# Optimization experiments

Measured on AMD Instinct MI355X. Metric: run time of the kernel, lower is better.

Reference implementation:

```python
import jax, jax.numpy as jnp
import numpy as np

B, L, E, D, T, NS, NSYM = 1024, 80, 256, 256, 20, 4, 100


def setup_inputs() -> dict:
    key = jax.random.key(0)
    ks = jax.random.split(key, 20)
    s = 0.05  # weight scale
    inp = {
        "encoder_outputs": jax.random.normal(ks[0], (B, L, E), jnp.float32),
        "symbols_encodings": jax.random.normal(ks[1], (B, NSYM, D), jnp.float32),
        "target_symbols_idxs": jax.random.randint(ks[2], (B, T), 0, NS + NSYM),
        "common_emb": jax.random.normal(ks[3], (NS, D), jnp.float32) * s,
        "W_attn": jax.random.normal(ks[4], (L, 2 * D), jnp.float32) * s,
        "b_attn": jnp.zeros((L,), jnp.float32),
        "W_comb": jax.random.normal(ks[5], (D, D + E), jnp.float32) * s,
        "b_comb": jnp.zeros((D,), jnp.float32),
        "Wih0": jax.random.normal(ks[6], (4 * D, D), jnp.float32) * s,
        "Whh0": jax.random.normal(ks[7], (4 * D, D), jnp.float32) * s,
        "bih0": jnp.zeros((4 * D,), jnp.float32),
        "bhh0": jnp.zeros((4 * D,), jnp.float32),
        "Wih1": jax.random.normal(ks[8], (4 * D, D), jnp.float32) * s,
        "Whh1": jax.random.normal(ks[9], (4 * D, D), jnp.float32) * s,
        "bih1": jnp.zeros((4 * D,), jnp.float32),
        "bhh1": jnp.zeros((4 * D,), jnp.float32),
        "W_out": jax.random.normal(ks[10], (D, E), jnp.float32) * s,
        "b_out": jnp.zeros((D,), jnp.float32),
    }
    return inp


def _lstm_cell(x, h, c, Wih, Whh, bih, bhh):
    # PyTorch gate order: i, f, g, o
    g = x @ Wih.T + h @ Whh.T + bih + bhh
    i, f, gg, o = jnp.split(g, 4, axis=-1)
    c = jax.nn.sigmoid(f) * c + jax.nn.sigmoid(i) * jnp.tanh(gg)
    h = jax.nn.sigmoid(o) * jnp.tanh(c)
    return h, c


def reference(encoder_outputs, symbols_encodings, target_symbols_idxs,
              common_emb, W_attn, b_attn, W_comb, b_comb,
              Wih0, Whh0, bih0, bhh0, Wih1, Whh1, bih1, bhh1,
              W_out, b_out):
    b, t = target_symbols_idxs.shape
    ns = common_emb.shape[0]
    nsym = symbols_encodings.shape[1]
    dt = encoder_outputs.dtype
    d = symbols_encodings.shape[-1]

    # apply_batched_embeddings: idx < ns -> common table, else per-example table
    idx = target_symbols_idxs
    special = common_emb[jnp.clip(idx, 0, ns - 1)]                      # [B,T,D]
    batched = jnp.take_along_axis(
        symbols_encodings, jnp.clip(idx - ns, 0, nsym - 1)[..., None], axis=1)  # [B,T,D]
    emb = jnp.where((idx < ns)[..., None], special, batched)            # [B,T,D]
    emb_t = jnp.swapaxes(emb, 0, 1)                                     # [T,B,D]

    def step(carry, e):
        h0, c0, h1, c1 = carry
        # Bahdanau-style attention over encoder positions
        aw = jnp.concatenate([e, h1], axis=1) @ W_attn.T + b_attn       # [B,L]
        ap = jax.nn.softmax(aw, axis=1)
        applied = jnp.einsum('bl,ble->be', ap, encoder_outputs)         # [B,E]
        comb = jax.nn.relu(jnp.concatenate([e, applied], axis=1) @ W_comb.T + b_comb)
        h0, c0 = _lstm_cell(comb, h0, c0, Wih0, Whh0, bih0, bhh0)
        h1, c1 = _lstm_cell(h0, h1, c1, Wih1, Whh1, bih1, bhh1)
        out = jax.nn.log_softmax(h1 @ W_out.T + b_out, axis=1)          # [B,D]
        return (h0, c0, h1, c1), out

    init = tuple(jnp.zeros((b, d), dt) for _ in range(4))
    _, outs = jax.lax.scan(step, init, emb_t)
    return outs  # [T,B,D] stacked per-timestep log-probs
```

## Files before the change

kernel.cpp:

```cpp
#include <hip/hip_runtime.h>

#define B_ 1024
#define L_ 80
#define E_ 256
#define D_ 256
#define T_ 20
#define NS_ 4
#define NSYM_ 100

typedef __attribute__((ext_vector_type(8))) short short8;
typedef __attribute__((ext_vector_type(4))) float f32x4;

__device__ inline short f2b(float f) {
    unsigned u = __float_as_uint(f);
    unsigned r = (u + 0x7fffu + ((u >> 16) & 1u)) >> 16;
    return (short)r;
}
__device__ inline float b2f(short s) {
    return __uint_as_float(((unsigned)(unsigned short)s) << 16);
}


__global__ void zero_k(unsigned* __restrict__ p, size_t n) {
    size_t i = (size_t)blockIdx.x * blockDim.x + threadIdx.x;
    size_t stride = (size_t)gridDim.x * blockDim.x;
    for (; i < n; i += stride) p[i] = 0u;
}

__global__ void f2b4_k(const float* __restrict__ src, short* __restrict__ dst, size_t n4) {
    size_t i = (size_t)blockIdx.x * blockDim.x + threadIdx.x;
    size_t stride = (size_t)gridDim.x * blockDim.x;
    for (; i < n4; i += stride) {
        float4 v = ((const float4*)src)[i];
        short4 o;
        o.x = f2b(v.x); o.y = f2b(v.y); o.z = f2b(v.z); o.w = f2b(v.w);
        ((short4*)dst)[i] = o;
    }
}

__global__ void split_k(const float* __restrict__ Wsrc, short* __restrict__ dstE,
                        short* __restrict__ dstH, int rows) {
    int id = blockIdx.x * 256 + threadIdx.x;
    if (id >= rows * 512) return;
    int rr = id >> 9, cc = id & 511;
    short v = f2b(Wsrc[id]);
    if (cc < 256) dstE[rr * 256 + cc] = v;
    else          dstH[rr * 256 + (cc - 256)] = v;
}

__global__ void gatesW_k(const float* __restrict__ Wih, const float* __restrict__ Whh,
                         const float* __restrict__ bih, const float* __restrict__ bhh,
                         short* __restrict__ WgB, float* __restrict__ bg) {
    int id = blockIdx.x * 256 + threadIdx.x;
    int np = id >> 9, cc = id & 511;
    int u = np >> 2, g = np & 3;
    int srow = g * 256 + u;
    float v = (cc < 256) ? Wih[srow * 256 + cc] : Whh[srow * 256 + (cc - 256)];
    WgB[id] = f2b(v);
    if (id < 1024) {
        int u2 = id >> 2, g2 = id & 3;
        bg[id] = bih[g2 * 256 + u2] + bhh[g2 * 256 + u2];
    }
}

__global__ void embed_k(const int* __restrict__ tsi, const float* __restrict__ common,
                        const float* __restrict__ syms, short* __restrict__ embB) {
    size_t id = (size_t)blockIdx.x * 256 + threadIdx.x;
    int d = (int)(id & 255);
    size_t r = id >> 8;
    int tt = (int)(r >> 10);
    int b  = (int)(r & 1023);
    int idx = tsi[b * T_ + tt];
    float v;
    if (idx < NS_) {
        int i2 = idx < 0 ? 0 : idx;
        v = common[i2 * D_ + d];
    } else {
        int i2 = idx - NS_;
        if (i2 > NSYM_ - 1) i2 = NSYM_ - 1;
        v = syms[((size_t)b * NSYM_ + i2) * D_ + d];
    }
    embB[id] = f2b(v);
}


__global__ __launch_bounds__(256) void gemm_k(
    const short* __restrict__ A, int lda,
    const short* __restrict__ W,
    const float* __restrict__ addend, int ldAdd,
    const float* __restrict__ bias,
    int act,
    float* __restrict__ outF, int ldoF,
    short* __restrict__ outB, int ldoB,
    int M, int N, int K)
{
    __shared__ alignas(16) short As[64][40];
    __shared__ alignas(16) short Ws[64][40];
    int m0 = blockIdx.x * 64, n0 = blockIdx.y * 64;
    int t = threadIdx.x;
    int w = t >> 6, l = t & 63, quad = l >> 4, lm = l & 15;
    int wm = (w >> 1) * 32, wn = (w & 1) * 32;
    f32x4 acc[2][2] = {};
    int rowL = t >> 2, c8 = (t & 3) * 8;
    for (int k0 = 0; k0 < K; k0 += 32) {
        uint4 av = *(const uint4*)(A + (size_t)(m0 + rowL) * lda + k0 + c8);
        uint4 wv = {0u, 0u, 0u, 0u};
        int wr = n0 + rowL;
        if (wr < N) wv = *(const uint4*)(W + (size_t)wr * K + k0 + c8);
        *(uint4*)&As[rowL][c8] = av;
        *(uint4*)&Ws[rowL][c8] = wv;
        __syncthreads();
        short8 af[2], wf[2];
        af[0] = *(const short8*)&As[wm + lm][quad * 8];
        af[1] = *(const short8*)&As[wm + 16 + lm][quad * 8];
        wf[0] = *(const short8*)&Ws[wn + lm][quad * 8];
        wf[1] = *(const short8*)&Ws[wn + 16 + lm][quad * 8];
        #pragma unroll
        for (int i = 0; i < 2; i++)
            #pragma unroll
            for (int j = 0; j < 2; j++)
                acc[i][j] = __builtin_amdgcn_mfma_f32_16x16x32_bf16(af[i], wf[j], acc[i][j], 0, 0, 0);
        __syncthreads();
    }
    #pragma unroll
    for (int i = 0; i < 2; i++)
        #pragma unroll
        for (int j = 0; j < 2; j++) {
            int col = n0 + wn + j * 16 + lm;
            if (col >= N) continue;
            float bval = bias ? bias[col] : 0.f;
            #pragma unroll
            for (int r = 0; r < 4; r++) {
                int row = m0 + wm + i * 16 + quad * 4 + r;
                float v = acc[i][j][r] + bval;
                if (addend) v += addend[(size_t)row * ldAdd + col];
                if (act == 1) v = fmaxf(v, 0.f);
                if (outF) outF[(size_t)row * ldoF + col] = v;
                if (outB) outB[(size_t)row * ldoB + col] = f2b(v);
            }
        }
}


__global__ __launch_bounds__(256) void fused_attn_comb_k(
    const short* __restrict__ h1B,
    const short* __restrict__ WaH,
    const float* __restrict__ awEt,
    const short* __restrict__ encW,
    const float* __restrict__ combEt,
    const float* __restrict__ b_comb,
    short* __restrict__ X0p)
{
    __shared__ float h1S[256];
    __shared__ float awS[80];
    __shared__ float apS[80];
    int b = blockIdx.x, t = threadIdx.x;
    h1S[t] = b2f(h1B[(size_t)b * 256 + t]);
    __syncthreads();
    float aw = 0.f;
    if (t < 80) {
        const short8* wp = (const short8*)(WaH + (size_t)t * 256);
        float acc = 0.f;
        #pragma unroll 4
        for (int k = 0; k < 32; k++) {
            short8 wv = wp[k];
            const float* hp = &h1S[k * 8];
            acc += hp[0] * b2f(wv[0]) + hp[1] * b2f(wv[1])
                 + hp[2] * b2f(wv[2]) + hp[3] * b2f(wv[3])
                 + hp[4] * b2f(wv[4]) + hp[5] * b2f(wv[5])
                 + hp[6] * b2f(wv[6]) + hp[7] * b2f(wv[7]);
        }
        aw = acc + awEt[(size_t)b * 80 + t];
        awS[t] = aw;
    }
    __syncthreads();
    float mx = -1e30f;
    #pragma unroll 8
    for (int i = 0; i < 80; i++) mx = fmaxf(mx, awS[i]);
    if (t < 80) apS[t] = __expf(aw - mx);
    __syncthreads();
    float s = 0.f;
    #pragma unroll 8
    for (int i = 0; i < 80; i++) s += apS[i];
    float inv = 1.f / s;
    const short* p = encW + (size_t)b * 80 * 256 + t;
    float acc = 0.f;
    #pragma unroll 8
    for (int l = 0; l < 80; l++) acc += apS[l] * b2f(p[(size_t)l * 256]);
    float v = acc * inv + combEt[(size_t)b * 256 + t] + b_comb[t];
    v = fmaxf(v, 0.f);
    X0p[(size_t)b * 512 + t] = f2b(v);
}


__global__ __launch_bounds__(256) void gates_lstm_k(
    const short* __restrict__ X,
    const short* __restrict__ Wg,
    const float* __restrict__ bg,
    float* __restrict__ c,
    short* __restrict__ hA, int ldA, int offA,
    short* __restrict__ hB2, int ldB2, int offB2)
{
    __shared__ alignas(16) short As[64][40];
    __shared__ alignas(16) short Ws[64][40];
    __shared__ float gS[64][68];
    int m0 = blockIdx.x * 64, n0 = blockIdx.y * 64;
    int t = threadIdx.x, w = t >> 6, l = t & 63, quad = l >> 4, lm = l & 15;
    int wm = (w >> 1) * 32, wn = (w & 1) * 32;
    f32x4 acc[2][2] = {};
    int rowL = t >> 2, c8 = (t & 3) * 8;
    for (int k0 = 0; k0 < 512; k0 += 32) {
        *(uint4*)&As[rowL][c8] = *(const uint4*)(X + (size_t)(m0 + rowL) * 512 + k0 + c8);
        *(uint4*)&Ws[rowL][c8] = *(const uint4*)(Wg + (size_t)(n0 + rowL) * 512 + k0 + c8);
        __syncthreads();
        short8 af[2], wf[2];
        af[0] = *(const short8*)&As[wm + lm][quad * 8];
        af[1] = *(const short8*)&As[wm + 16 + lm][quad * 8];
        wf[0] = *(const short8*)&Ws[wn + lm][quad * 8];
        wf[1] = *(const short8*)&Ws[wn + 16 + lm][quad * 8];
        #pragma unroll
        for (int i = 0; i < 2; i++)
            #pragma unroll
            for (int j = 0; j < 2; j++)
                acc[i][j] = __builtin_amdgcn_mfma_f32_16x16x32_bf16(af[i], wf[j], acc[i][j], 0, 0, 0);
        __syncthreads();
    }
    #pragma unroll
    for (int i = 0; i < 2; i++)
        #pragma unroll
        for (int j = 0; j < 2; j++) {
            int col = wn + j * 16 + lm;
            float bval = bg[n0 + col];
            #pragma unroll
            for (int r = 0; r < 4; r++)
                gS[wm + i * 16 + quad * 4 + r][col] = acc[i][j][r] + bval;
        }
    __syncthreads();
    int U0 = n0 >> 2;
    for (int item = t; item < 1024; item += 256) {
        int ml = item >> 4, ul = item & 15;
        float iv = gS[ml][ul * 4 + 0];
        float fv = gS[ml][ul * 4 + 1];
        float gv = gS[ml][ul * 4 + 2];
        float ov = gS[ml][ul * 4 + 3];
        float si = 1.f / (1.f + __expf(-iv));
        float sf = 1.f / (1.f + __expf(-fv));
        float so = 1.f / (1.f + __expf(-ov));
        float tg = tanhf(gv);
        int m = m0 + ml, u = U0 + ul;
        size_t ci = (size_t)m * 256 + u;
        float cn = sf * c[ci] + si * tg;
        float hn = so * tanhf(cn);
        c[ci] = cn;
        short hb = f2b(hn);
        hA[(size_t)m * ldA + offA + u] = hb;
        hB2[(size_t)m * ldB2 + offB2 + u] = hb;
    }
}


__global__ __launch_bounds__(256) void out_k(
    const short* __restrict__ h1B,
    const short* __restrict__ WoB,
    const float* __restrict__ b_out,
    float* __restrict__ outT)
{
    __shared__ alignas(16) short As[32][40];
    __shared__ alignas(16) short Ws[256][40];
    __shared__ float oS[32][260];
    int m0 = blockIdx.x * 32;
    int t = threadIdx.x, w = t >> 6, l = t & 63, quad = l >> 4, lm = l & 15;
    int wm = (w >> 1) * 16, wn = (w & 1) * 128;
    f32x4 acc[8] = {};
    for (int k0 = 0; k0 < 256; k0 += 32) {
        if (t < 128) {
            int rr = t >> 2, cc = (t & 3) * 8;
            *(uint4*)&As[rr][cc] = *(const uint4*)(h1B + (size_t)(m0 + rr) * 256 + k0 + cc);
        }
        for (int cch = t; cch < 1024; cch += 256) {
            int rr = cch >> 2, cc = (cch & 3) * 8;
            *(uint4*)&Ws[rr][cc] = *(const uint4*)(WoB + (size_t)rr * 256 + k0 + cc);
        }
        __syncthreads();
        short8 af = *(const short8*)&As[wm + lm][quad * 8];
        #pragma unroll
        for (int j = 0; j < 8; j++) {
            short8 wf = *(const short8*)&Ws[wn + j * 16 + lm][quad * 8];
            acc[j] = __builtin_amdgcn_mfma_f32_16x16x32_bf16(af, wf, acc[j], 0, 0, 0);
        }
        __syncthreads();
    }
    #pragma unroll
    for (int j = 0; j < 8; j++)
        #pragma unroll
        for (int r = 0; r < 4; r++)
            oS[wm + quad * 4 + r][wn + j * 16 + lm] = acc[j][r] + b_out[wn + j * 16 + lm];
    __syncthreads();
    int row = t >> 3, q = t & 7;
    float mx = -1e30f;
    for (int i = q * 32; i < q * 32 + 32; i++) mx = fmaxf(mx, oS[row][i]);
    mx = fmaxf(mx, __shfl_xor(mx, 1));
    mx = fmaxf(mx, __shfl_xor(mx, 2));
    mx = fmaxf(mx, __shfl_xor(mx, 4));
    float s = 0.f;
    for (int i = q * 32; i < q * 32 + 32; i++) s += __expf(oS[row][i] - mx);
    s += __shfl_xor(s, 1); s += __shfl_xor(s, 2); s += __shfl_xor(s, 4);
    float lg = mx + logf(s);
    float* orow = outT + (size_t)(m0 + row) * 256;
    for (int i = q * 32; i < q * 32 + 32; i++) orow[i] = oS[row][i] - lg;
}


extern "C" void kernel_launch(void* const* d_in, const int* in_sizes, int n_in,
                              void* d_out, int out_size, void* d_ws, size_t ws_size,
                              hipStream_t stream) {
    const float* encF    = (const float*)d_in[0];
    const float* syms    = (const float*)d_in[1];
    const int*   tsi     = (const int*)d_in[2];
    const float* commonE = (const float*)d_in[3];
    const float* W_attn  = (const float*)d_in[4];
    const float* b_attn  = (const float*)d_in[5];
    const float* W_comb  = (const float*)d_in[6];
    const float* b_comb  = (const float*)d_in[7];
    const float* Wih0    = (const float*)d_in[8];
    const float* Whh0    = (const float*)d_in[9];
    const float* bih0    = (const float*)d_in[10];
    const float* bhh0    = (const float*)d_in[11];
    const float* Wih1    = (const float*)d_in[12];
    const float* Whh1    = (const float*)d_in[13];
    const float* bih1    = (const float*)d_in[14];
    const float* bhh1    = (const float*)d_in[15];
    const float* W_out   = (const float*)d_in[16];
    const float* b_out   = (const float*)d_in[17];
    float* out = (float*)d_out;

    char* base = (char*)d_ws;
    size_t off = 0;
    auto alloc = [&](size_t bytes) -> char* {
        char* p = base + off;
        off += (bytes + 255) & ~(size_t)255;
        return p;
    };
    float* c0    = (float*)alloc((size_t)B_ * D_ * 4);
    float* c1    = (float*)alloc((size_t)B_ * D_ * 4);
    short* X0a   = (short*)alloc((size_t)B_ * 512 * 2);
    short* X1a   = (short*)alloc((size_t)B_ * 512 * 2);
    short* H1all = (short*)alloc((size_t)(T_ + 1) * B_ * D_ * 2);
    size_t zeroBytes = (size_t)((char*)H1all - base) + (size_t)B_ * D_ * 2;
    short* X0b   = (short*)alloc((size_t)B_ * 512 * 2);
    short* X1b   = (short*)alloc((size_t)B_ * 512 * 2);
    float* awE   = (float*)alloc((size_t)T_ * B_ * L_ * 4);
    float* combE = (float*)alloc((size_t)T_ * B_ * D_ * 4);
    short* embB  = (short*)alloc((size_t)T_ * B_ * D_ * 2);
    short* WaEB  = (short*)alloc((size_t)L_ * D_ * 2);
    short* WaHB  = (short*)alloc((size_t)L_ * D_ * 2);
    short* WcEB  = (short*)alloc((size_t)D_ * D_ * 2);
    short* WcAB  = (short*)alloc((size_t)D_ * E_ * 2);
    short* Wg0B  = (short*)alloc((size_t)1024 * 512 * 2);
    short* Wg1B  = (short*)alloc((size_t)1024 * 512 * 2);
    short* WoutB = (short*)alloc((size_t)D_ * E_ * 2);
    float* bg0   = (float*)alloc(1024 * 4);
    float* bg1   = (float*)alloc(1024 * 4);
    short* encB  = (short*)alloc((size_t)B_ * L_ * E_ * 2);
    short* encW  = (short*)alloc((size_t)B_ * L_ * D_ * 2);
    (void)encF; (void)ws_size; (void)in_sizes; (void)n_in; (void)out_size;

    zero_k<<<2048, 256, 0, stream>>>((unsigned*)base, zeroBytes / 4);
    f2b4_k<<<4096, 256, 0, stream>>>(encF, encB, (size_t)B_ * L_ * E_ / 4);
    f2b4_k<<<64, 256, 0, stream>>>(W_out, WoutB, (size_t)D_ * E_ / 4);
    split_k<<<(80 * 512) / 256, 256, 0, stream>>>(W_attn, WaEB, WaHB, 80);
    split_k<<<(256 * 512) / 256, 256, 0, stream>>>(W_comb, WcEB, WcAB, 256);
    gatesW_k<<<2048, 256, 0, stream>>>(Wih0, Whh0, bih0, bhh0, Wg0B, bg0);
    gatesW_k<<<2048, 256, 0, stream>>>(Wih1, Whh1, bih1, bhh1, Wg1B, bg1);
    embed_k<<<(T_ * B_ * D_) / 256, 256, 0, stream>>>(tsi, commonE, syms, embB);
    gemm_k<<<dim3(320, 2), 256, 0, stream>>>(embB, 256, WaEB, nullptr, 0, b_attn, 0,
                                             awE, 80, nullptr, 0, 20480, 80, 256);
    gemm_k<<<dim3(320, 4), 256, 0, stream>>>(embB, 256, WcEB, nullptr, 0, nullptr, 0,
                                             combE, 256, nullptr, 0, 20480, 256, 256);
    gemm_k<<<dim3(1280, 4), 256, 0, stream>>>(encB, 256, WcAB, nullptr, 0, nullptr, 0,
                                              nullptr, 0, encW, 256, 81920, 256, 256);

    for (int tt = 0; tt < T_; tt++) {
        int p = tt & 1;
        short* X0p = p ? X0b : X0a;
        short* X0q = p ? X0a : X0b;
        short* X1p = p ? X1b : X1a;
        short* X1q = p ? X1a : X1b;

        fused_attn_comb_k<<<1024, 256, 0, stream>>>(
            H1all + (size_t)tt * B_ * D_, WaHB, awE + (size_t)tt * B_ * L_,
            encW, combE + (size_t)tt * B_ * D_, b_comb, X0p);
        gates_lstm_k<<<dim3(16, 16), 256, 0, stream>>>(X0p, Wg0B, bg0, c0,
                                                       X0q, 512, 256, X1p, 512, 0);
        gates_lstm_k<<<dim3(16, 16), 256, 0, stream>>>(X1p, Wg1B, bg1, c1,
                                                       X1q, 512, 256,
                                                       H1all + (size_t)(tt + 1) * B_ * D_, 256, 0);
    }
    out_k<<<640, 256, 0, stream>>>(H1all + (size_t)B_ * D_, WoutB, b_out, out);
}
```

Before: 1.082 ms.

## Fuse decoder time loop into one persistent kernel with on-chip LSTM state

Replaces the per-timestep launches (attention/combine plus two LSTM gate kernels, 60 launches) with one persistent kernel. Each of 64 blocks owns 16 batch rows for all 20 steps. The LSTM cell states stay in registers and the hidden and input vectors stay in LDS, so the global zeroing kernel and the intermediate round-trips through memory go away. The attention score projection now uses MFMA, and the comb bias is folded into the precomputed GEMM. The cost is that only 64 workgroups run, far fewer than the CUs available, and every block streams the full gate weight matrices from L2 at every step, so the kernel may become limited by per-CU bandwidth.

```diff
diff --git a/kernel.cpp b/kernel.cpp
--- a/kernel.cpp
+++ b/kernel.cpp
@@ -8,6 +8,11 @@
 #define NS_ 4
 #define NSYM_ 100
 
+#define ROWS 16
+#define NBLK 64
+#define XP 520
+#define GP 260
+
 typedef __attribute__((ext_vector_type(8))) short short8;
 typedef __attribute__((ext_vector_type(4))) float f32x4;
 
@@ -20,12 +25,6 @@
     return __uint_as_float(((unsigned)(unsigned short)s) << 16);
 }
 
-
-__global__ void zero_k(unsigned* __restrict__ p, size_t n) {
-    size_t i = (size_t)blockIdx.x * blockDim.x + threadIdx.x;
-    size_t stride = (size_t)gridDim.x * blockDim.x;
-    for (; i < n; i += stride) p[i] = 0u;
-}
 
 __global__ void f2b4_k(const float* __restrict__ src, short* __restrict__ dst, size_t n4) {
     size_t i = (size_t)blockIdx.x * blockDim.x + threadIdx.x;
@@ -142,119 +141,152 @@
 }
 
 
-__global__ __launch_bounds__(256) void fused_attn_comb_k(
-    const short* __restrict__ h1B,
-    const short* __restrict__ WaH,
-    const float* __restrict__ awEt,
-    const short* __restrict__ encW,
-    const float* __restrict__ combEt,
-    const float* __restrict__ b_comb,
-    short* __restrict__ X0p)
-{
-    __shared__ float h1S[256];
-    __shared__ float awS[80];
-    __shared__ float apS[80];
-    int b = blockIdx.x, t = threadIdx.x;
-    h1S[t] = b2f(h1B[(size_t)b * 256 + t]);
-    __syncthreads();
-    float aw = 0.f;
-    if (t < 80) {
-        const short8* wp = (const short8*)(WaH + (size_t)t * 256);
-        float acc = 0.f;
-        #pragma unroll 4
-        for (int k = 0; k < 32; k++) {
-            short8 wv = wp[k];
-            const float* hp = &h1S[k * 8];
-            acc += hp[0] * b2f(wv[0]) + hp[1] * b2f(wv[1])
-                 + hp[2] * b2f(wv[2]) + hp[3] * b2f(wv[3])
-                 + hp[4] * b2f(wv[4]) + hp[5] * b2f(wv[5])
-                 + hp[6] * b2f(wv[6]) + hp[7] * b2f(wv[7]);
-        }
-        aw = acc + awEt[(size_t)b * 80 + t];
-        awS[t] = aw;
-    }
-    __syncthreads();
-    float mx = -1e30f;
-    #pragma unroll 8
-    for (int i = 0; i < 80; i++) mx = fmaxf(mx, awS[i]);
-    if (t < 80) apS[t] = __expf(aw - mx);
-    __syncthreads();
-    float s = 0.f;
-    #pragma unroll 8
-    for (int i = 0; i < 80; i++) s += apS[i];
-    float inv = 1.f / s;
-    const short* p = encW + (size_t)b * 80 * 256 + t;
-    float acc = 0.f;
-    #pragma unroll 8
-    for (int l = 0; l < 80; l++) acc += apS[l] * b2f(p[(size_t)l * 256]);
-    float v = acc * inv + combEt[(size_t)b * 256 + t] + b_comb[t];
-    v = fmaxf(v, 0.f);
-    X0p[(size_t)b * 512 + t] = f2b(v);
-}
-
-
-__global__ __launch_bounds__(256) void gates_lstm_k(
-    const short* __restrict__ X,
+struct DecArgs {
+    short* H1all;
+    const short* WaHB;
+    const float* awE;
+    const short* encW;
+    const float* combE;
+    const short* Wg0; const float* bg0;
+    const short* Wg1; const float* bg1;
+};
+
+__device__ inline void layer_lstm(
+    const short (*X)[XP],
     const short* __restrict__ Wg,
     const float* __restrict__ bg,
-    float* __restrict__ c,
-    short* __restrict__ hA, int ldA, int offA,
-    short* __restrict__ hB2, int ldB2, int offB2)
+    float* creg,
+    float (*gSv)[GP],
+    short (*Hd1)[XP], int off1,
+    short (*Hd2)[XP], int off2,
+    short* __restrict__ gdst,
+    int w, int l, int quad, int lm)
 {
-    __shared__ alignas(16) short As[64][40];
-    __shared__ alignas(16) short Ws[64][40];
-    __shared__ float gS[64][68];
-    int m0 = blockIdx.x * 64, n0 = blockIdx.y * 64;
+    f32x4 acc[16] = {};
+    #pragma unroll 4
+    for (int k0s = 0; k0s < 16; k0s++) {
+        int k0 = k0s * 32;
+        short8 af = *(const short8*)&X[lm][k0 + quad * 8];
+        #pragma unroll
+        for (int j = 0; j < 16; j++) {
+            short8 wf = *(const short8*)(Wg + (size_t)(w * 256 + j * 16 + lm) * 512 + k0 + quad * 8);
+            acc[j] = __builtin_amdgcn_mfma_f32_16x16x32_bf16(af, wf, acc[j], 0, 0, 0);
+        }
+    }
+    __syncthreads();
+    #pragma unroll
+    for (int j = 0; j < 16; j++) {
+        float bv = bg[w * 256 + j * 16 + lm];
+        #pragma unroll
+        for (int r = 0; r < 4; r++)
+            gSv[quad * 4 + r][j * 16 + lm] = acc[j][r] + bv;
+    }
+    int u = w * 64 + l;
+    #pragma unroll
+    for (int row = 0; row < ROWS; row++) {
+        float4 g4 = *(const float4*)&gSv[row][l * 4];
+        float si = 1.f / (1.f + __expf(-g4.x));
+        float sf = 1.f / (1.f + __expf(-g4.y));
+        float tg = 2.f / (1.f + __expf(-2.f * g4.z)) - 1.f;
+        float so = 1.f / (1.f + __expf(-g4.w));
+        float cn = sf * creg[row] + si * tg;
+        creg[row] = cn;
+        float hn = so * (2.f / (1.f + __expf(-2.f * cn)) - 1.f);
+        short hb = f2b(hn);
+        Hd1[row][off1 + u] = hb;
+        if (Hd2) Hd2[row][off2 + u] = hb;
+        if (gdst) gdst[(size_t)row * 256 + u] = hb;
+    }
+    __syncthreads();
+}
+
+__global__ __launch_bounds__(256, 1) void decode_k(DecArgs a)
+{
+    __shared__ short X0[ROWS][XP];
+    __shared__ short X1[ROWS][XP];
+    __shared__ float gS[4][ROWS][GP];
+    __shared__ float awS[ROWS][80];
+    __shared__ float apS[ROWS][80];
+
     int t = threadIdx.x, w = t >> 6, l = t & 63, quad = l >> 4, lm = l & 15;
-    int wm = (w >> 1) * 32, wn = (w & 1) * 32;
-    f32x4 acc[2][2] = {};
-    int rowL = t >> 2, c8 = (t & 3) * 8;
-    for (int k0 = 0; k0 < 512; k0 += 32) {
-        *(uint4*)&As[rowL][c8] = *(const uint4*)(X + (size_t)(m0 + rowL) * 512 + k0 + c8);
-        *(uint4*)&Ws[rowL][c8] = *(const uint4*)(Wg + (size_t)(n0 + rowL) * 512 + k0 + c8);
-        __syncthreads();
-        short8 af[2], wf[2];
-        af[0] = *(const short8*)&As[wm + lm][quad * 8];
-        af[1] = *(const short8*)&As[wm + 16 + lm][quad * 8];
-        wf[0] = *(const short8*)&Ws[wn + lm][quad * 8];
-        wf[1] = *(const short8*)&Ws[wn + 16 + lm][quad * 8];
-        #pragma unroll
-        for (int i = 0; i < 2; i++)
-            #pragma unroll
-            for (int j = 0; j < 2; j++)
-                acc[i][j] = __builtin_amdgcn_mfma_f32_16x16x32_bf16(af[i], wf[j], acc[i][j], 0, 0, 0);
-        __syncthreads();
-    }
+    int b0 = blockIdx.x * ROWS;
+
+    for (int i = t; i < ROWS * XP; i += 256) { (&X0[0][0])[i] = 0; (&X1[0][0])[i] = 0; }
+    float c0r[ROWS], c1r[ROWS];
     #pragma unroll
-    for (int i = 0; i < 2; i++)
-        #pragma unroll
-        for (int j = 0; j < 2; j++) {
-            int col = wn + j * 16 + lm;
-            float bval = bg[n0 + col];
-            #pragma unroll
-            for (int r = 0; r < 4; r++)
-                gS[wm + i * 16 + quad * 4 + r][col] = acc[i][j][r] + bval;
-        }
+    for (int i = 0; i < ROWS; i++) { c0r[i] = 0.f; c1r[i] = 0.f; }
     __syncthreads();
-    int U0 = n0 >> 2;
-    for (int item = t; item < 1024; item += 256) {
-        int ml = item >> 4, ul = item & 15;
-        float iv = gS[ml][ul * 4 + 0];
-        float fv = gS[ml][ul * 4 + 1];
-        float gv = gS[ml][ul * 4 + 2];
-        float ov = gS[ml][ul * 4 + 3];
-        float si = 1.f / (1.f + __expf(-iv));
-        float sf = 1.f / (1.f + __expf(-fv));
-        float so = 1.f / (1.f + __expf(-ov));
-        float tg = tanhf(gv);
-        int m = m0 + ml, u = U0 + ul;
-        size_t ci = (size_t)m * 256 + u;
-        float cn = sf * c[ci] + si * tg;
-        float hn = so * tanhf(cn);
-        c[ci] = cn;
-        short hb = f2b(hn);
-        hA[(size_t)m * ldA + offA + u] = hb;
-        hB2[(size_t)m * ldB2 + offB2 + u] = hb;
+
+    for (int tt = 0; tt < T_; tt++) {
+        {
+            f32x4 acc0 = {}, acc1 = {};
+            #pragma unroll
+            for (int ks = 0; ks < 8; ks++) {
+                int k0 = ks * 32 + quad * 8;
+                short8 af = *(const short8*)&X1[lm][256 + k0];
+                short8 wf0 = *(const short8*)(a.WaHB + (size_t)(w * 16 + lm) * 256 + k0);
+                acc0 = __builtin_amdgcn_mfma_f32_16x16x32_bf16(af, wf0, acc0, 0, 0, 0);
+                if (w == 0) {
+                    short8 wf1 = *(const short8*)(a.WaHB + (size_t)(64 + lm) * 256 + k0);
+                    acc1 = __builtin_amdgcn_mfma_f32_16x16x32_bf16(af, wf1, acc1, 0, 0, 0);
+                }
+            }
+            const float* awEt = a.awE + ((size_t)tt * B_ + b0) * 80;
+            #pragma unroll
+            for (int r = 0; r < 4; r++) {
+                int row = quad * 4 + r;
+                awS[row][w * 16 + lm] = acc0[r] + awEt[(size_t)row * 80 + w * 16 + lm];
+                if (w == 0)
+                    awS[row][64 + lm] = acc1[r] + awEt[(size_t)row * 80 + 64 + lm];
+            }
+        }
+        __syncthreads();
+        {
+            int row = w * 4 + quad;
+            float v[5];
+            float mx = -1e30f;
+            #pragma unroll
+            for (int j = 0; j < 5; j++) { v[j] = awS[row][lm + 16 * j]; mx = fmaxf(mx, v[j]); }
+            #pragma unroll
+            for (int d = 1; d < 16; d <<= 1) mx = fmaxf(mx, __shfl_xor(mx, d));
+            float s = 0.f;
+            #pragma unroll
+            for (int j = 0; j < 5; j++) { v[j] = __expf(v[j] - mx); s += v[j]; }
+            #pragma unroll
+            for (int d = 1; d < 16; d <<= 1) s += __shfl_xor(s, d);
+            float inv = 1.f / s;
+            #pragma unroll
+            for (int j = 0; j < 5; j++) apS[row][lm + 16 * j] = v[j] * inv;
+        }
+        {
+            #pragma unroll
+            for (int r_ = 0; r_ < 4; r_++) {
+                int row = w * 4 + r_;
+                int b = b0 + row;
+                const short* ep = a.encW + ((size_t)b * 80) * 256 + l * 4;
+                float o0 = 0.f, o1 = 0.f, o2 = 0.f, o3 = 0.f;
+                #pragma unroll 8
+                for (int ll = 0; ll < 80; ll++) {
+                    float apv = apS[row][ll];
+                    short4 ev = *(const short4*)(ep + (size_t)ll * 256);
+                    o0 += apv * b2f(ev.x); o1 += apv * b2f(ev.y);
+                    o2 += apv * b2f(ev.z); o3 += apv * b2f(ev.w);
+                }
+                float4 cE = *(const float4*)(a.combE + ((size_t)tt * B_ + b) * 256 + l * 4);
+                short4 ov;
+                ov.x = f2b(fmaxf(o0 + cE.x, 0.f));
+                ov.y = f2b(fmaxf(o1 + cE.y, 0.f));
+                ov.z = f2b(fmaxf(o2 + cE.z, 0.f));
+                ov.w = f2b(fmaxf(o3 + cE.w, 0.f));
+                *(short4*)&X0[row][l * 4] = ov;
+            }
+        }
+        __syncthreads();
+        layer_lstm(X0, a.Wg0, a.bg0, c0r, gS[w],
+                   X1, 0, X0, 256, nullptr, w, l, quad, lm);
+        layer_lstm(X1, a.Wg1, a.bg1, c1r, gS[w],
+                   X1, 256, nullptr, 0,
+                   a.H1all + ((size_t)(tt + 1) * B_ + b0) * 256, w, l, quad, lm);
     }
 }
 
@@ -341,14 +373,7 @@
         off += (bytes + 255) & ~(size_t)255;
         return p;
     };
-    float* c0    = (float*)alloc((size_t)B_ * D_ * 4);
-    float* c1    = (float*)alloc((size_t)B_ * D_ * 4);
-    short* X0a   = (short*)alloc((size_t)B_ * 512 * 2);
-    short* X1a   = (short*)alloc((size_t)B_ * 512 * 2);
     short* H1all = (short*)alloc((size_t)(T_ + 1) * B_ * D_ * 2);
-    size_t zeroBytes = (size_t)((char*)H1all - base) + (size_t)B_ * D_ * 2;
-    short* X0b   = (short*)alloc((size_t)B_ * 512 * 2);
-    short* X1b   = (short*)alloc((size_t)B_ * 512 * 2);
     float* awE   = (float*)alloc((size_t)T_ * B_ * L_ * 4);
     float* combE = (float*)alloc((size_t)T_ * B_ * D_ * 4);
     short* embB  = (short*)alloc((size_t)T_ * B_ * D_ * 2);
@@ -363,9 +388,8 @@
     float* bg1   = (float*)alloc(1024 * 4);
     short* encB  = (short*)alloc((size_t)B_ * L_ * E_ * 2);
     short* encW  = (short*)alloc((size_t)B_ * L_ * D_ * 2);
-    (void)encF; (void)ws_size; (void)in_sizes; (void)n_in; (void)out_size;
-
-    zero_k<<<2048, 256, 0, stream>>>((unsigned*)base, zeroBytes / 4);
+    (void)ws_size; (void)in_sizes; (void)n_in; (void)out_size;
+
     f2b4_k<<<4096, 256, 0, stream>>>(encF, encB, (size_t)B_ * L_ * E_ / 4);
     f2b4_k<<<64, 256, 0, stream>>>(W_out, WoutB, (size_t)D_ * E_ / 4);
     split_k<<<(80 * 512) / 256, 256, 0, stream>>>(W_attn, WaEB, WaHB, 80);
@@ -375,26 +399,16 @@
     embed_k<<<(T_ * B_ * D_) / 256, 256, 0, stream>>>(tsi, commonE, syms, embB);
     gemm_k<<<dim3(320, 2), 256, 0, stream>>>(embB, 256, WaEB, nullptr, 0, b_attn, 0,
                                              awE, 80, nullptr, 0, 20480, 80, 256);
-    gemm_k<<<dim3(320, 4), 256, 0, stream>>>(embB, 256, WcEB, nullptr, 0, nullptr, 0,
+    gemm_k<<<dim3(320, 4), 256, 0, stream>>>(embB, 256, WcEB, nullptr, 0, b_comb, 0,
                                              combE, 256, nullptr, 0, 20480, 256, 256);
     gemm_k<<<dim3(1280, 4), 256, 0, stream>>>(encB, 256, WcAB, nullptr, 0, nullptr, 0,
                                               nullptr, 0, encW, 256, 81920, 256, 256);
 
-    for (int tt = 0; tt < T_; tt++) {
-        int p = tt & 1;
-        short* X0p = p ? X0b : X0a;
-        short* X0q = p ? X0a : X0b;
-        short* X1p = p ? X1b : X1a;
-        short* X1q = p ? X1a : X1b;
-
-        fused_attn_comb_k<<<1024, 256, 0, stream>>>(
-            H1all + (size_t)tt * B_ * D_, WaHB, awE + (size_t)tt * B_ * L_,
-            encW, combE + (size_t)tt * B_ * D_, b_comb, X0p);
-        gates_lstm_k<<<dim3(16, 16), 256, 0, stream>>>(X0p, Wg0B, bg0, c0,
-                                                       X0q, 512, 256, X1p, 512, 0);
-        gates_lstm_k<<<dim3(16, 16), 256, 0, stream>>>(X1p, Wg1B, bg1, c1,
-                                                       X1q, 512, 256,
-                                                       H1all + (size_t)(tt + 1) * B_ * D_, 256, 0);
-    }
+    DecArgs da;
+    da.H1all = H1all; da.WaHB = WaHB; da.awE = awE; da.encW = encW; da.combE = combE;
+    da.Wg0 = Wg0B; da.bg0 = bg0;
+    da.Wg1 = Wg1B; da.bg1 = bg1;
+    decode_k<<<NBLK, 256, 0, stream>>>(da);
+
     out_k<<<640, 256, 0, stream>>>(H1all + (size_t)B_ * D_, WoutB, b_out, out);
 }
```

New measurement: 2.974 ms. +174.8%, slower.
